# Optimization experiments

Measured on AMD Instinct MI355X. Metric: run time of the kernel, lower is better.

The kernel has to match this reference:

```python
import jax, jax.numpy as jnp
import numpy as np
import math

B, S, D = 4, 2048, 768
H = 12
DH = D // H  # 64
NEG = -1e10

def setup_inputs() -> dict:
    key = jax.random.key(0)
    ks = jax.random.split(key, 8)
    scale = 0.02
    return {
        "hidden_states": jax.random.normal(ks[0], (B, S, D), dtype=jnp.float32),
        "attention_mask": jnp.zeros((B, 1, 1, S), dtype=jnp.float32),
        "Wq": jax.random.normal(ks[1], (D, D), dtype=jnp.float32) * scale,
        "bq": jnp.zeros((D,), dtype=jnp.float32),
        "Wk": jax.random.normal(ks[2], (D, D), dtype=jnp.float32) * scale,
        "bk": jnp.zeros((D,), dtype=jnp.float32),
        "Wv": jax.random.normal(ks[3], (D, D), dtype=jnp.float32) * scale,
        "bv": jnp.zeros((D,), dtype=jnp.float32),
    }

def reference(hidden_states, attention_mask, Wq, bq, Wk, bk, Wv, bv):
    # Linear projections; note attention_mask is accepted but unused, matching the torch module.
    def split_heads(x):  # [B,S,D] -> [B,H,S,DH]
        return x.reshape(B, S, H, DH).transpose(0, 2, 1, 3)
    q = split_heads(hidden_states @ Wq + bq)
    k = split_heads(hidden_states @ Wk + bk)
    v = split_heads(hidden_states @ Wv + bv)
    scores = jnp.einsum("bhqd,bhkd->bhqk", q, k) / math.sqrt(DH)
    causal = jnp.tril(jnp.ones((S, S), dtype=bool))  # masked_fill(mask==0, -1e10)
    scores = jnp.where(causal, scores, NEG)
    probs = jax.nn.softmax(scores, axis=-1)
    # dropout prob = 0.0 (eval) -> identity
    ctx = jnp.einsum("bhqk,bhkd->bhqd", probs, v)
    return ctx.transpose(0, 2, 1, 3).reshape(B, S, D)
```

## Files before the change

kernel.cpp:

```cpp
#include <hip/hip_runtime.h>
#include <hip/hip_bf16.h>

#define B_  4
#define S_  2048
#define D_  768
#define H_  12
#define DH_ 64

typedef __bf16 bf16;
typedef __attribute__((ext_vector_type(8))) __bf16 bf16x8;
typedef __attribute__((ext_vector_type(4))) __bf16 bf16x4;
typedef __attribute__((ext_vector_type(4))) float floatx4;
typedef __attribute__((ext_vector_type(16))) float floatx16;

__device__ __forceinline__ int chunk_off2(int qt2) {
    if (qt2 < 4)  return qt2;
    if (qt2 < 8)  return 4 + 2 * (qt2 - 4);
    if (qt2 < 12) return 12 + 3 * (qt2 - 8);
    return 24 + 4 * (qt2 - 12);
}

__device__ __forceinline__ unsigned pack_bf16(float a, float b) {
    unsigned short ua = __builtin_bit_cast(unsigned short, (bf16)a);
    unsigned short ub = __builtin_bit_cast(unsigned short, (bf16)b);
    return (unsigned)ua | ((unsigned)ub << 16);
}

__global__ __launch_bounds__(256) void cvt_f32_bf16(const float* __restrict__ in,
                                                    bf16* __restrict__ out, int n4) {
    int i = blockIdx.x * 256 + threadIdx.x;
    if (i < n4) {
        float4 v = ((const float4*)in)[i];
        bf16x4 o;
        o[0] = (bf16)v.x; o[1] = (bf16)v.y; o[2] = (bf16)v.z; o[3] = (bf16)v.w;
        *(bf16x4*)(out + (size_t)i * 4) = o;
    }
}

__global__ __launch_bounds__(256) void w_transpose(const float* __restrict__ w0,
                                                   const float* __restrict__ w1,
                                                   const float* __restrict__ w2,
                                                   bf16* __restrict__ Wt)
{
    const int which = blockIdx.z;
    const float* W = (which == 0) ? w0 : (which == 1 ? w1 : w2);
    bf16* dst = Wt + (size_t)which * D_ * D_;
    __shared__ bf16 t[64 * 72];
    const int k0 = blockIdx.x * 64, n0 = blockIdx.y * 64;
    const int tid = threadIdx.x;
    {
        int r = tid >> 2;
        int c0 = (tid & 3) * 16;
        #pragma unroll
        for (int q = 0; q < 4; q++) {
            float4 v = *(const float4*)(W + (size_t)(k0 + r) * D_ + n0 + c0 + q * 4);
            t[(c0 + q * 4 + 0) * 72 + r] = (bf16)v.x;
            t[(c0 + q * 4 + 1) * 72 + r] = (bf16)v.y;
            t[(c0 + q * 4 + 2) * 72 + r] = (bf16)v.z;
            t[(c0 + q * 4 + 3) * 72 + r] = (bf16)v.w;
        }
    }
    __syncthreads();
    {
        int n = tid >> 3, seg = tid & 7;
        *(bf16x8*)(dst + (size_t)(n0 + n) * D_ + k0 + seg * 8) =
            *(const bf16x8*)(t + n * 72 + seg * 8);
        *(bf16x8*)(dst + (size_t)(n0 + n + 32) * D_ + k0 + seg * 8) =
            *(const bf16x8*)(t + (n + 32) * 72 + seg * 8);
    }
}

__global__ __launch_bounds__(256) void qkv_gemm(
    const bf16* __restrict__ Xb, const bf16* __restrict__ Wt,
    const float* __restrict__ bq, const float* __restrict__ bk,
    const float* __restrict__ bv, bf16* __restrict__ QKV)
{
    const int which = blockIdx.z;
    const bf16* Wm = Wt + (size_t)which * D_ * D_;
    const float* bias = (which == 0) ? bq : (which == 1 ? bk : bv);
    bf16* out = QKV + (size_t)which * B_ * H_ * S_ * DH_;

    __shared__ bf16 As[128 * 72];
    __shared__ bf16 Bs[128 * 72];

    const int tid  = threadIdx.x;
    const int wave = tid >> 6, lane = tid & 63;
    const int wr = wave >> 1, wc = wave & 1;
    const int g = lane >> 4, ln = lane & 15;
    const int m0 = blockIdx.x * 128, n0 = blockIdx.y * 128;

    floatx4 acc[4][4];
    #pragma unroll
    for (int i = 0; i < 4; i++)
        #pragma unroll
        for (int j = 0; j < 4; j++)
            acc[i][j] = (floatx4){0.f, 0.f, 0.f, 0.f};

    int row_[4], seg_[4];
    #pragma unroll
    for (int t = 0; t < 4; t++) { int fc = tid + t * 256; row_[t] = fc >> 3; seg_[t] = fc & 7; }

    bf16x8 apf[4], bpf[4];
    #pragma unroll
    for (int t = 0; t < 4; t++) {
        apf[t] = *(const bf16x8*)(Xb + (size_t)(m0 + row_[t]) * D_ + seg_[t] * 8);
        bpf[t] = *(const bf16x8*)(Wm + (size_t)(n0 + row_[t]) * D_ + seg_[t] * 8);
    }

    for (int k0 = 0; k0 < D_; k0 += 64) {
        __syncthreads();
        #pragma unroll
        for (int t = 0; t < 4; t++) {
            *(bf16x8*)(As + row_[t] * 72 + seg_[t] * 8) = apf[t];
            *(bf16x8*)(Bs + row_[t] * 72 + seg_[t] * 8) = bpf[t];
        }
        __syncthreads();
        if (k0 + 64 < D_) {
            #pragma unroll
            for (int t = 0; t < 4; t++) {
                apf[t] = *(const bf16x8*)(Xb + (size_t)(m0 + row_[t]) * D_ + k0 + 64 + seg_[t] * 8);
                bpf[t] = *(const bf16x8*)(Wm + (size_t)(n0 + row_[t]) * D_ + k0 + 64 + seg_[t] * 8);
            }
        }
        #pragma unroll
        for (int ks = 0; ks < 2; ks++) {
            bf16x8 af[4], bfr[4];
            #pragma unroll
            for (int i = 0; i < 4; i++)
                af[i] = *(const bf16x8*)(As + (wr * 64 + i * 16 + ln) * 72 + ks * 32 + g * 8);
            #pragma unroll
            for (int j = 0; j < 4; j++)
                bfr[j] = *(const bf16x8*)(Bs + (wc * 64 + j * 16 + ln) * 72 + ks * 32 + g * 8);
            #pragma unroll
            for (int i = 0; i < 4; i++)
                #pragma unroll
                for (int j = 0; j < 4; j++)
                    acc[i][j] = __builtin_amdgcn_mfma_f32_16x16x32_bf16(af[i], bfr[j], acc[i][j], 0, 0, 0);
        }
    }

    const float sc = (which == 0) ? 0.125f : 1.0f;
    #pragma unroll
    for (int i = 0; i < 4; i++) {
        #pragma unroll
        for (int j = 0; j < 4; j++) {
            int col = n0 + wc * 64 + j * 16 + ln;
            float bv_ = bias[col];
            int h = col >> 6, dh = col & 63;
            int rowbase = m0 + wr * 64 + i * 16 + g * 4;
            int b = rowbase >> 11, s0 = rowbase & 2047;
            if (which == 2) {
                bf16x4 o;
                #pragma unroll
                for (int r = 0; r < 4; r++) o[r] = (bf16)(acc[i][j][r] + bv_);
                *(bf16x4*)(out + ((size_t)((b * H_ + h) * DH_ + dh)) * S_ + s0) = o;
            } else {
                #pragma unroll
                for (int r = 0; r < 4; r++)
                    out[(((size_t)(b * H_ + h) * S_ + s0 + r) << 6) + dh] =
                        (bf16)((acc[i][j][r] + bv_) * sc);
            }
        }
    }
}

__global__ __launch_bounds__(256) void attn_chunk(const bf16* __restrict__ QKV,
                                                  float* __restrict__ out,
                                                  bf16* __restrict__ Opart,
                                                  float* __restrict__ Lpart)
{
    const int cid = 39 - blockIdx.x;
    const int bh = blockIdx.y;
    const int b = bh / H_, h = bh % H_;

    int qt2, c;
    if (cid < 4)       { qt2 = cid; c = 0; }
    else if (cid < 12) { int t = cid - 4;  qt2 = 4 + (t >> 1);  c = t & 1; }
    else if (cid < 24) { int t = cid - 12; qt2 = 8 + t / 3;     c = t - 3 * (t / 3); }
    else               { int t = cid - 24; qt2 = 12 + (t >> 2); c = t & 3; }
    const int nch = (2 * qt2 + 9) >> 3;
    const int kt0 = c * 8;
    const int kt1 = min(kt0 + 7, 2 * qt2 + 1);

    const size_t MAT = (size_t)B_ * H_ * S_ * DH_;
    const bf16* Q  = QKV +           (size_t)bh * S_ * DH_;
    const bf16* K  = QKV + MAT +     (size_t)bh * S_ * DH_;
    const bf16* Vt = QKV + 2 * MAT + (size_t)bh * S_ * DH_;

    __shared__ bf16 Ks[64 * 72];
    __shared__ bf16 Vts[64 * 72];

    const int tid  = threadIdx.x;
    const int wave = tid >> 6, lane = tid & 63;
    const int l31 = lane & 31, lh = lane >> 5;
    const int srow = tid >> 3, sseg = tid & 7;
    const int qbase = qt2 * 128;
    const int qs = qbase + wave * 32;
    const int q = qs + l31;

    bf16x8 qf[4];
    {
        const bf16* qrow = Q + (size_t)q * DH_ + lh * 8;
        #pragma unroll
        for (int s = 0; s < 4; s++) qf[s] = *(const bf16x8*)(qrow + s * 16);
    }

    floatx16 accO[2];
    #pragma unroll
    for (int dt = 0; dt < 2; dt++)
        #pragma unroll
        for (int e = 0; e < 16; e++) accO[dt][e] = 0.f;
    float Lrun = 0.f;

    const bf16* kptr = K  + (size_t)(kt0 * 64 + srow) * DH_ + sseg * 8;
    const bf16* vptr = Vt + (size_t)srow * S_ + kt0 * 64 + sseg * 8;
    bf16x8 ka = *(const bf16x8*)kptr;
    bf16x8 kb = *(const bf16x8*)(kptr + 32 * DH_);
    bf16x8 va = *(const bf16x8*)vptr;
    bf16x8 vb = *(const bf16x8*)(vptr + (size_t)32 * S_);

    for (int kt = kt0; kt <= kt1; ++kt) {
        __syncthreads();
        *(bf16x8*)(Ks  + srow * 72 + sseg * 8) = ka;
        *(bf16x8*)(Ks  + (srow + 32) * 72 + sseg * 8) = kb;
        *(bf16x8*)(Vts + srow * 72 + sseg * 8) = va;
        *(bf16x8*)(Vts + (srow + 32) * 72 + sseg * 8) = vb;
        __syncthreads();
        if (kt < kt1) {
            kptr += 64 * DH_;
            vptr += 64;
            ka = *(const bf16x8*)kptr;
            kb = *(const bf16x8*)(kptr + 32 * DH_);
            va = *(const bf16x8*)vptr;
            vb = *(const bf16x8*)(vptr + (size_t)32 * S_);
        }

        floatx16 accS[2];
        #pragma unroll
        for (int kk = 0; kk < 2; kk++) {
            #pragma unroll
            for (int e = 0; e < 16; e++) accS[kk][e] = 0.f;
            #pragma unroll
            for (int s = 0; s < 4; s++) {
                bf16x8 kf = *(const bf16x8*)(Ks + (kk * 32 + l31) * 72 + s * 16 + lh * 8);
                accS[kk] = __builtin_amdgcn_mfma_f32_32x32x16_bf16(kf, qf[s], accS[kk], 0, 0, 0);
            }
        }

        unsigned pk1[2][4], pk2[2][4];
        const bool domask = (kt * 64 + 63 > qs);
        #pragma unroll
        for (int kk = 0; kk < 2; kk++) {
            const int keyb = kt * 64 + kk * 32 + 4 * lh;
            #pragma unroll
            for (int rq = 0; rq < 4; rq++) {
                float p[4];
                #pragma unroll
                for (int rr = 0; rr < 4; rr++) {
                    float v = __expf(accS[kk][4 * rq + rr]);
                    if (domask && (keyb + 8 * rq + rr > q)) v = 0.f;
                    p[rr] = v;
                    Lrun += v;
                }
                pk1[kk][rq] = pack_bf16(p[0], p[1]);
                pk2[kk][rq] = pack_bf16(p[2], p[3]);
            }
        }

        #pragma unroll
        for (int s = 0; s < 4; s++) {
            const int kk = s >> 1, sl = s & 1;
            unsigned sendA = lh ? pk1[kk][2 * sl] : pk1[kk][2 * sl + 1];
            unsigned sendB = lh ? pk2[kk][2 * sl] : pk2[kk][2 * sl + 1];
            unsigned recvA = __shfl_xor(sendA, 32, 64);
            unsigned recvB = __shfl_xor(sendB, 32, 64);
            uint4 w;
            w.x = lh ? recvA : pk1[kk][2 * sl];
            w.y = lh ? recvB : pk2[kk][2 * sl];
            w.z = lh ? pk1[kk][2 * sl + 1] : recvA;
            w.w = lh ? pk2[kk][2 * sl + 1] : recvB;
            bf16x8 ptf = __builtin_bit_cast(bf16x8, w);
            #pragma unroll
            for (int dt = 0; dt < 2; dt++) {
                bf16x8 vf = *(const bf16x8*)(Vts + (dt * 32 + l31) * 72 + s * 16 + lh * 8);
                accO[dt] = __builtin_amdgcn_mfma_f32_32x32x16_bf16(vf, ptf, accO[dt], 0, 0, 0);
            }
        }
    }

    const float L = Lrun + __shfl_xor(Lrun, 32, 64);

    if (nch == 1) {
        const float inv = 1.0f / L;
        float* orow = out + (size_t)(b * S_ + q) * D_ + h * DH_;
        #pragma unroll
        for (int dt = 0; dt < 2; dt++)
            #pragma unroll
            for (int rq = 0; rq < 4; rq++) {
                float4 o;
                o.x = accO[dt][4 * rq + 0] * inv; o.y = accO[dt][4 * rq + 1] * inv;
                o.z = accO[dt][4 * rq + 2] * inv; o.w = accO[dt][4 * rq + 3] * inv;
                *(float4*)(orow + dt * 32 + 8 * rq + 4 * lh) = o;
            }
    } else {
        const int chunk = bh * 40 + chunk_off2(qt2) + c;
        bf16* obase = Opart + (size_t)chunk * 8192 + (wave * 32 + l31) * 64;
        #pragma unroll
        for (int dt = 0; dt < 2; dt++)
            #pragma unroll
            for (int rq = 0; rq < 4; rq++) {
                bf16x4 o;
                #pragma unroll
                for (int rr = 0; rr < 4; rr++) o[rr] = (bf16)accO[dt][4 * rq + rr];
                *(bf16x4*)(obase + dt * 32 + 8 * rq + 4 * lh) = o;
            }
        if (lh == 0) Lpart[chunk * 128 + wave * 32 + l31] = L;
    }
}

__global__ __launch_bounds__(256) void attn_reduce(const bf16* __restrict__ Opart,
                                                   const float* __restrict__ Lpart,
                                                   float* __restrict__ out)
{
    const int qt2 = 4 + blockIdx.x;
    const int bh = blockIdx.y;
    const int b = bh / H_, h = bh % H_;
    const int nch = (2 * qt2 + 9) >> 3;
    const int cb = bh * 40 + chunk_off2(qt2);

    const int e = threadIdx.x;
    const int ql = e >> 1, dh0 = (e & 1) * 32;

    float o[32];
    #pragma unroll
    for (int i = 0; i < 32; i++) o[i] = 0.f;
    float l = 0.f;

    for (int cidx = 0; cidx < nch; cidx++) {
        const bf16* p = Opart + (size_t)(cb + cidx) * 8192 + ql * 64 + dh0;
        #pragma unroll
        for (int m = 0; m < 4; m++) {
            bf16x8 v = *(const bf16x8*)(p + m * 8);
            #pragma unroll
            for (int k = 0; k < 8; k++) o[m * 8 + k] += (float)v[k];
        }
        l += Lpart[(cb + cidx) * 128 + ql];
    }
    float inv = 1.0f / l;
    float* orow = out + (size_t)(b * S_ + qt2 * 128 + ql) * D_ + h * DH_ + dh0;
    #pragma unroll
    for (int m = 0; m < 8; m++) {
        float4 v;
        v.x = o[m * 4 + 0] * inv; v.y = o[m * 4 + 1] * inv;
        v.z = o[m * 4 + 2] * inv; v.w = o[m * 4 + 3] * inv;
        *(float4*)(orow + m * 4) = v;
    }
}

extern "C" void kernel_launch(void* const* d_in, const int* in_sizes, int n_in,
                              void* d_out, int out_size, void* d_ws, size_t ws_size,
                              hipStream_t stream) {
    const float* hs = (const float*)d_in[0];
    const float* Wq = (const float*)d_in[2];
    const float* bq = (const float*)d_in[3];
    const float* Wk = (const float*)d_in[4];
    const float* bk = (const float*)d_in[5];
    const float* Wv = (const float*)d_in[6];
    const float* bv = (const float*)d_in[7];
    float* out = (float*)d_out;

    bf16* Xb    = (bf16*)d_ws;
    bf16* Wt    = Xb + (size_t)8192 * 768;
    bf16* QKV   = Wt + (size_t)3 * 768 * 768;
    bf16* Opart = QKV + (size_t)3 * B_ * H_ * S_ * DH_;
    float* Lpart = (float*)(Opart + (size_t)1920 * 8192);

    cvt_f32_bf16<<<6144, 256, 0, stream>>>(hs, Xb, 1572864);
    w_transpose<<<dim3(12, 12, 3), 256, 0, stream>>>(Wq, Wk, Wv, Wt);
    qkv_gemm<<<dim3(64, 6, 3), 256, 0, stream>>>(Xb, Wt, bq, bk, bv, QKV);
    attn_chunk<<<dim3(40, 48), 256, 0, stream>>>(QKV, out, Opart, Lpart);
    attn_reduce<<<dim3(12, 48), 256, 0, stream>>>(Opart, Lpart, out);
}
```

Before: 207.0 us.

## Use direct global-to-LDS loads with XOR swizzle in QKV GEMM, streamline attention softmax

The QKV GEMM now fills shared memory with global_load_lds instead of register prefetch plus LDS stores. It switches from padded rows to an XOR-swizzled unpadded layout to avoid bank conflicts, but loses the register-level prefetch overlap. The attention kernel gets an occupancy hint of 3 blocks per SM and splits the causal-mask branch so unmasked tiles skip the per-element compare. It also interleaves the S computation with the PV MFMAs per 32-key half to cut live registers, uses a cheaper round-half-up bf16 pack, and keeps split partial row sums.

```diff
diff --git a/kernel.cpp b/kernel.cpp
--- a/kernel.cpp
+++ b/kernel.cpp
@@ -13,17 +13,22 @@
 typedef __attribute__((ext_vector_type(4))) float floatx4;
 typedef __attribute__((ext_vector_type(16))) float floatx16;
 
+__device__ __forceinline__ void load_lds16(const bf16* g, bf16* l) {
+    __builtin_amdgcn_global_load_lds((const __attribute__((address_space(1))) void*)g,
+                                     (__attribute__((address_space(3))) void*)l, 16, 0, 0);
+}
+
+__device__ __forceinline__ unsigned pack2(float a, float b) {
+    unsigned ua = __builtin_bit_cast(unsigned, a) + 0x8000u;
+    unsigned ub = __builtin_bit_cast(unsigned, b) + 0x8000u;
+    return __builtin_amdgcn_perm(ub, ua, 0x07060302);
+}
+
 __device__ __forceinline__ int chunk_off2(int qt2) {
     if (qt2 < 4)  return qt2;
     if (qt2 < 8)  return 4 + 2 * (qt2 - 4);
     if (qt2 < 12) return 12 + 3 * (qt2 - 8);
     return 24 + 4 * (qt2 - 12);
-}
-
-__device__ __forceinline__ unsigned pack_bf16(float a, float b) {
-    unsigned short ua = __builtin_bit_cast(unsigned short, (bf16)a);
-    unsigned short ub = __builtin_bit_cast(unsigned short, (bf16)b);
-    return (unsigned)ua | ((unsigned)ub << 16);
 }
 
 __global__ __launch_bounds__(256) void cvt_f32_bf16(const float* __restrict__ in,
@@ -80,14 +85,15 @@
     const float* bias = (which == 0) ? bq : (which == 1 ? bk : bv);
     bf16* out = QKV + (size_t)which * B_ * H_ * S_ * DH_;
 
-    __shared__ bf16 As[128 * 72];
-    __shared__ bf16 Bs[128 * 72];
+    __shared__ bf16 As[128 * 64];
+    __shared__ bf16 Bs[128 * 64];
 
     const int tid  = threadIdx.x;
     const int wave = tid >> 6, lane = tid & 63;
     const int wr = wave >> 1, wc = wave & 1;
     const int g = lane >> 4, ln = lane & 15;
     const int m0 = blockIdx.x * 128, n0 = blockIdx.y * 128;
+    const int fbase = wave * 256 + lane;
 
     floatx4 acc[4][4];
     #pragma unroll
@@ -96,41 +102,27 @@
         for (int j = 0; j < 4; j++)
             acc[i][j] = (floatx4){0.f, 0.f, 0.f, 0.f};
 
-    int row_[4], seg_[4];
-    #pragma unroll
-    for (int t = 0; t < 4; t++) { int fc = tid + t * 256; row_[t] = fc >> 3; seg_[t] = fc & 7; }
-
-    bf16x8 apf[4], bpf[4];
-    #pragma unroll
-    for (int t = 0; t < 4; t++) {
-        apf[t] = *(const bf16x8*)(Xb + (size_t)(m0 + row_[t]) * D_ + seg_[t] * 8);
-        bpf[t] = *(const bf16x8*)(Wm + (size_t)(n0 + row_[t]) * D_ + seg_[t] * 8);
-    }
-
     for (int k0 = 0; k0 < D_; k0 += 64) {
         __syncthreads();
         #pragma unroll
-        for (int t = 0; t < 4; t++) {
-            *(bf16x8*)(As + row_[t] * 72 + seg_[t] * 8) = apf[t];
-            *(bf16x8*)(Bs + row_[t] * 72 + seg_[t] * 8) = bpf[t];
+        for (int i = 0; i < 4; i++) {
+            int fc = fbase + i * 64;
+            int row = fc >> 3;
+            int seg = (fc & 7) ^ (row & 7);
+            load_lds16(Xb + (size_t)(m0 + row) * D_ + k0 + seg * 8, As + fc * 8);
+            load_lds16(Wm + (size_t)(n0 + row) * D_ + k0 + seg * 8, Bs + fc * 8);
         }
         __syncthreads();
-        if (k0 + 64 < D_) {
-            #pragma unroll
-            for (int t = 0; t < 4; t++) {
-                apf[t] = *(const bf16x8*)(Xb + (size_t)(m0 + row_[t]) * D_ + k0 + 64 + seg_[t] * 8);
-                bpf[t] = *(const bf16x8*)(Wm + (size_t)(n0 + row_[t]) * D_ + k0 + 64 + seg_[t] * 8);
-            }
-        }
         #pragma unroll
         for (int ks = 0; ks < 2; ks++) {
+            const int sx = ((ks * 4 + g) ^ (ln & 7)) * 8;
             bf16x8 af[4], bfr[4];
             #pragma unroll
             for (int i = 0; i < 4; i++)
-                af[i] = *(const bf16x8*)(As + (wr * 64 + i * 16 + ln) * 72 + ks * 32 + g * 8);
+                af[i] = *(const bf16x8*)(As + ((wr * 64 + i * 16 + ln) << 6) + sx);
             #pragma unroll
             for (int j = 0; j < 4; j++)
-                bfr[j] = *(const bf16x8*)(Bs + (wc * 64 + j * 16 + ln) * 72 + ks * 32 + g * 8);
+                bfr[j] = *(const bf16x8*)(Bs + ((wc * 64 + j * 16 + ln) << 6) + sx);
             #pragma unroll
             for (int i = 0; i < 4; i++)
                 #pragma unroll
@@ -164,10 +156,10 @@
     }
 }
 
-__global__ __launch_bounds__(256) void attn_chunk(const bf16* __restrict__ QKV,
-                                                  float* __restrict__ out,
-                                                  bf16* __restrict__ Opart,
-                                                  float* __restrict__ Lpart)
+__global__ __launch_bounds__(256, 3) void attn_chunk(const bf16* __restrict__ QKV,
+                                                     float* __restrict__ out,
+                                                     bf16* __restrict__ Opart,
+                                                     float* __restrict__ Lpart)
 {
     const int cid = 39 - blockIdx.x;
     const int bh = blockIdx.y;
@@ -210,7 +202,7 @@
     for (int dt = 0; dt < 2; dt++)
         #pragma unroll
         for (int e = 0; e < 16; e++) accO[dt][e] = 0.f;
-    float Lrun = 0.f;
+    float lsum[4] = {0.f, 0.f, 0.f, 0.f};
 
     const bf16* kptr = K  + (size_t)(kt0 * 64 + srow) * DH_ + sseg * 8;
     const bf16* vptr = Vt + (size_t)srow * S_ + kt0 * 64 + sseg * 8;
@@ -235,60 +227,74 @@
             vb = *(const bf16x8*)(vptr + (size_t)32 * S_);
         }
 
-        floatx16 accS[2];
+        const bool domask = (kt * 64 + 63 > qs);
+
         #pragma unroll
         for (int kk = 0; kk < 2; kk++) {
-            #pragma unroll
-            for (int e = 0; e < 16; e++) accS[kk][e] = 0.f;
+            floatx16 accS;
+            #pragma unroll
+            for (int e = 0; e < 16; e++) accS[e] = 0.f;
             #pragma unroll
             for (int s = 0; s < 4; s++) {
                 bf16x8 kf = *(const bf16x8*)(Ks + (kk * 32 + l31) * 72 + s * 16 + lh * 8);
-                accS[kk] = __builtin_amdgcn_mfma_f32_32x32x16_bf16(kf, qf[s], accS[kk], 0, 0, 0);
-            }
-        }
-
-        unsigned pk1[2][4], pk2[2][4];
-        const bool domask = (kt * 64 + 63 > qs);
-        #pragma unroll
-        for (int kk = 0; kk < 2; kk++) {
-            const int keyb = kt * 64 + kk * 32 + 4 * lh;
-            #pragma unroll
-            for (int rq = 0; rq < 4; rq++) {
-                float p[4];
-                #pragma unroll
-                for (int rr = 0; rr < 4; rr++) {
-                    float v = __expf(accS[kk][4 * rq + rr]);
-                    if (domask && (keyb + 8 * rq + rr > q)) v = 0.f;
-                    p[rr] = v;
-                    Lrun += v;
+                accS = __builtin_amdgcn_mfma_f32_32x32x16_bf16(kf, qf[s], accS, 0, 0, 0);
+            }
+
+            unsigned pk1[4], pk2[4];
+            if (domask) {
+                const int keyb = kt * 64 + kk * 32 + 4 * lh;
+                #pragma unroll
+                for (int rq = 0; rq < 4; rq++) {
+                    float p[4];
+                    #pragma unroll
+                    for (int rr = 0; rr < 4; rr++) {
+                        float v = __expf(accS[4 * rq + rr]);
+                        if (keyb + 8 * rq + rr > q) v = 0.f;
+                        p[rr] = v;
+                        lsum[rq] += v;
+                    }
+                    pk1[rq] = pack2(p[0], p[1]);
+                    pk2[rq] = pack2(p[2], p[3]);
                 }
-                pk1[kk][rq] = pack_bf16(p[0], p[1]);
-                pk2[kk][rq] = pack_bf16(p[2], p[3]);
-            }
-        }
-
-        #pragma unroll
-        for (int s = 0; s < 4; s++) {
-            const int kk = s >> 1, sl = s & 1;
-            unsigned sendA = lh ? pk1[kk][2 * sl] : pk1[kk][2 * sl + 1];
-            unsigned sendB = lh ? pk2[kk][2 * sl] : pk2[kk][2 * sl + 1];
-            unsigned recvA = __shfl_xor(sendA, 32, 64);
-            unsigned recvB = __shfl_xor(sendB, 32, 64);
-            uint4 w;
-            w.x = lh ? recvA : pk1[kk][2 * sl];
-            w.y = lh ? recvB : pk2[kk][2 * sl];
-            w.z = lh ? pk1[kk][2 * sl + 1] : recvA;
-            w.w = lh ? pk2[kk][2 * sl + 1] : recvB;
-            bf16x8 ptf = __builtin_bit_cast(bf16x8, w);
-            #pragma unroll
-            for (int dt = 0; dt < 2; dt++) {
-                bf16x8 vf = *(const bf16x8*)(Vts + (dt * 32 + l31) * 72 + s * 16 + lh * 8);
-                accO[dt] = __builtin_amdgcn_mfma_f32_32x32x16_bf16(vf, ptf, accO[dt], 0, 0, 0);
-            }
-        }
-    }
-
-    const float L = Lrun + __shfl_xor(Lrun, 32, 64);
+            } else {
+                #pragma unroll
+                for (int rq = 0; rq < 4; rq++) {
+                    float p[4];
+                    #pragma unroll
+                    for (int rr = 0; rr < 4; rr++) {
+                        float v = __expf(accS[4 * rq + rr]);
+                        p[rr] = v;
+                        lsum[rq] += v;
+                    }
+                    pk1[rq] = pack2(p[0], p[1]);
+                    pk2[rq] = pack2(p[2], p[3]);
+                }
+            }
+
+            #pragma unroll
+            for (int sl = 0; sl < 2; sl++) {
+                const int s = kk * 2 + sl;
+                unsigned sendA = lh ? pk1[2 * sl] : pk1[2 * sl + 1];
+                unsigned sendB = lh ? pk2[2 * sl] : pk2[2 * sl + 1];
+                unsigned recvA = __shfl_xor(sendA, 32, 64);
+                unsigned recvB = __shfl_xor(sendB, 32, 64);
+                uint4 w;
+                w.x = lh ? recvA : pk1[2 * sl];
+                w.y = lh ? recvB : pk2[2 * sl];
+                w.z = lh ? pk1[2 * sl + 1] : recvA;
+                w.w = lh ? pk2[2 * sl + 1] : recvB;
+                bf16x8 ptf = __builtin_bit_cast(bf16x8, w);
+                #pragma unroll
+                for (int dt = 0; dt < 2; dt++) {
+                    bf16x8 vf = *(const bf16x8*)(Vts + (dt * 32 + l31) * 72 + s * 16 + lh * 8);
+                    accO[dt] = __builtin_amdgcn_mfma_f32_32x32x16_bf16(vf, ptf, accO[dt], 0, 0, 0);
+                }
+            }
+        }
+    }
+
+    const float Lr = (lsum[0] + lsum[1]) + (lsum[2] + lsum[3]);
+    const float L = Lr + __shfl_xor(Lr, 32, 64);
 
     if (nch == 1) {
         const float inv = 1.0f / L;
```

After: 202.9 us. No clear change (-1.9%).
